# Kernel optimization log

Hardware: AMD Instinct MI355X
Metric: run time of the kernel (lower is better)

The kernel has to match this reference:

```python
import jax, jax.numpy as jnp
import numpy as np

B = 512          # number of (query, corpus) pairs
MAX_SET = 128    # max_set_size
D_IN, E_IN = 32, 16
D = 128          # node_state_dim == filters_3
E_ENC = 64
M_HID = 256
T_DIM = 128      # transform_dim
N_PROP = 5
SINKHORN_ITERS = 20
TEMP = 0.1
DEG = 8


def setup_inputs() -> dict:
    key = jax.random.key(0)
    ks = jax.random.split(key, 16)
    # alternating graph sizes: query 128/64, corpus 64/128
    qsizes = np.where(np.arange(B) % 2 == 0, 128, 64).astype(np.int32)
    csizes = np.where(np.arange(B) % 2 == 0, 64, 128).astype(np.int32)
    sizes_flat = np.stack([qsizes, csizes], 1).reshape(-1)        # [2B] interleaved q,c
    N = int(sizes_flat.sum())                                     # 98304
    E = DEG * N                                                   # 786432
    starts = np.concatenate([[0], np.cumsum(sizes_flat)[:-1]])
    graph_idx = np.repeat(np.arange(2 * B), sizes_flat).astype(np.int32)
    rng = np.random.default_rng(0)
    from_idx = rng.integers(0, N, E).astype(np.int64)
    g = graph_idx[from_idx]                                       # keep edges within a graph
    to_idx = (starts[g] + rng.integers(0, 1 << 30, E) % sizes_flat[g]).astype(np.int64)

    def W(k, shape):
        s = 1.0 / np.sqrt(shape[0])
        return jax.random.uniform(k, shape, jnp.float32, -s, s)

    return dict(
        node_features=jax.random.normal(ks[0], (N, D_IN), jnp.float32),
        edge_features=jax.random.normal(ks[1], (E, E_IN), jnp.float32),
        enc_node_w=W(ks[2], (D_IN, D)), enc_node_b=jnp.zeros((D,), jnp.float32),
        enc_edge_w=W(ks[3], (E_IN, E_ENC)), enc_edge_b=jnp.zeros((E_ENC,), jnp.float32),
        msg_w1=W(ks[4], (2 * D + E_ENC, M_HID)), msg_b1=jnp.zeros((M_HID,), jnp.float32),
        msg_w2=W(ks[5], (M_HID, D)), msg_b2=jnp.zeros((D,), jnp.float32),
        rmsg_w1=W(ks[6], (2 * D + E_ENC, M_HID)), rmsg_b1=jnp.zeros((M_HID,), jnp.float32),
        rmsg_w2=W(ks[7], (M_HID, D)), rmsg_b2=jnp.zeros((D,), jnp.float32),
        upd_w1=W(ks[8], (2 * D, M_HID)), upd_b1=jnp.zeros((M_HID,), jnp.float32),
        upd_w2=W(ks[9], (M_HID, D)), upd_b2=jnp.zeros((D,), jnp.float32),
        fc1_w=W(ks[10], (D, T_DIM)), fc1_b=jnp.zeros((T_DIM,), jnp.float32),
        fc2_w=W(ks[11], (T_DIM, T_DIM)), fc2_b=jnp.zeros((T_DIM,), jnp.float32),
        from_idx=jnp.asarray(from_idx, jnp.int32),
        to_idx=jnp.asarray(to_idx, jnp.int32),
        graph_idx=jnp.asarray(graph_idx, jnp.int32),
        qsizes=jnp.asarray(qsizes, jnp.int32),
        csizes=jnp.asarray(csizes, jnp.int32),
    )


def _mlp2(x, w1, b1, w2, b2):
    return jax.nn.relu(x @ w1 + b1) @ w2 + b2


def reference(node_features, edge_features, enc_node_w, enc_node_b, enc_edge_w, enc_edge_b,
              msg_w1, msg_b1, msg_w2, msg_b2, rmsg_w1, rmsg_b1, rmsg_w2, rmsg_b2,
              upd_w1, upd_b1, upd_w2, upd_b2, fc1_w, fc1_b, fc2_w, fc2_b,
              from_idx, to_idx, graph_idx, qsizes, csizes):
    N = node_features.shape[0]
    # GraphEncoder: linear MLPs on node / edge features
    h = node_features @ enc_node_w + enc_node_b                   # [N, D]
    e = edge_features @ enc_edge_w + enc_edge_b                   # [E, E_ENC]
    # GraphPropLayer applied n_prop_layers times (shared params)
    for _ in range(N_PROP):
        src, dst = h[from_idx], h[to_idx]
        m = _mlp2(jnp.concatenate([src, dst, e], -1), msg_w1, msg_b1, msg_w2, msg_b2)
        agg = jax.ops.segment_sum(m, to_idx, num_segments=N)
        mr = _mlp2(jnp.concatenate([dst, src, e], -1), rmsg_w1, rmsg_b1, rmsg_w2, rmsg_b2)
        agg = agg + jax.ops.segment_sum(mr, from_idx, num_segments=N)
        h = h + _mlp2(jnp.concatenate([agg, h], -1), upd_w1, upd_b1, upd_w2, upd_b2)
    # split into per-graph chunks and pad to MAX_SET (scatter by (pair, side, position))
    sizes_flat = jnp.stack([qsizes, csizes], 1).reshape(-1)       # [2B]
    starts = jnp.concatenate([jnp.zeros((1,), sizes_flat.dtype), jnp.cumsum(sizes_flat)[:-1]])
    pos = jnp.arange(N, dtype=jnp.int32) - starts[graph_idx]
    pair, side = graph_idx // 2, graph_idx % 2
    stacked = jnp.zeros((B, 2, MAX_SET, D), h.dtype).at[pair, side, pos].set(h)
    stacked_q, stacked_c = stacked[:, 0], stacked[:, 1]           # [B, MAX_SET, D]
    # masked transform
    tq = _mlp2(stacked_q, fc1_w, fc1_b, fc2_w, fc2_b)
    tc = _mlp2(stacked_c, fc1_w, fc1_b, fc2_w, fc2_b)
    ar = jnp.arange(MAX_SET)
    qmask = (ar[None, :] < qsizes[:, None]).astype(h.dtype)[:, :, None]
    cmask = (ar[None, :] < csizes[:, None]).astype(h.dtype)[:, :, None]
    mq, mc = qmask * tq, cmask * tc
    # sinkhorn (noise_factor = 0, temperature = 0.1, 20 iters)
    log_alpha = jnp.einsum('bqd,bcd->bqc', mq, mc) / TEMP         # [B, MAX_SET, MAX_SET]
    for _ in range(SINKHORN_ITERS):
        log_alpha = log_alpha - jax.scipy.special.logsumexp(log_alpha, axis=2, keepdims=True)
        log_alpha = log_alpha - jax.scipy.special.logsumexp(log_alpha, axis=1, keepdims=True)
    plan = jnp.exp(log_alpha)
    # masked residual score
    scores = -jnp.sum(jax.nn.relu(stacked_q - plan @ stacked_c), axis=(1, 2))  # [B]
    return scores
```

## Files before the change

kernel.cpp:

```cpp
#include <hip/hip_runtime.h>

using bf16x8 = __attribute__((ext_vector_type(8))) __bf16;
using u16x8  = __attribute__((ext_vector_type(8))) unsigned short;
using f32x4  = __attribute__((ext_vector_type(4))) float;
using f32x2  = __attribute__((ext_vector_type(2))) float;

#define DEV static __device__ __forceinline__

constexpr int NN = 98304;
constexpr int NE = 786432;
constexpr int NB = 512;

constexpr size_t OFF_HB  = 0;
constexpr size_t OFF_AGG = OFF_HB + (size_t)NN*128*2;
constexpr size_t OFF_TH  = OFF_AGG;
constexpr size_t OFF_TL  = OFF_AGG + (size_t)NN*128*2;
constexpr size_t OFF_W   = OFF_AGG + (size_t)NN*128*4;

constexpr size_t WO_W1TM = 0;
constexpr size_t WO_W1TR = WO_W1TM + (size_t)81920*2;
constexpr size_t WO_W2TM = WO_W1TR + (size_t)81920*2;
constexpr size_t WO_W2TR = WO_W2TM + (size_t)32768*2;
constexpr size_t WO_W1TU = WO_W2TR + (size_t)32768*2;
constexpr size_t WO_W2TU = WO_W1TU + (size_t)65536*2;
constexpr size_t WO_WNT  = WO_W2TU + (size_t)32768*2;
constexpr size_t WO_WETP = WO_WNT  + (size_t)4096*2;
constexpr size_t WO_FC1F = WO_WETP + (size_t)2048*2;
constexpr size_t WO_FC2F = WO_FC1F + (size_t)16384*4;
constexpr size_t WO_BNF  = WO_FC2F + (size_t)16384*4;
constexpr size_t WO_BEF  = WO_BNF + 128*4;
constexpr size_t WO_B1M  = WO_BEF + 64*4;
constexpr size_t WO_B2M  = WO_B1M + 256*4;
constexpr size_t WO_B1R  = WO_B2M + 128*4;
constexpr size_t WO_B2R  = WO_B1R + 256*4;
constexpr size_t WO_B1U  = WO_B2R + 128*4;
constexpr size_t WO_B2U  = WO_B1U + 256*4;
constexpr size_t WO_FC1B = WO_B2U + 128*4;
constexpr size_t WO_FC2B = WO_FC1B + 128*4;
constexpr size_t WO_FLAG = WO_FC2B + 128*4;
constexpr size_t WO_END  = WO_FLAG + 16;

constexpr size_t OFF_HL  = OFF_W + WO_END;
constexpr size_t WS_MINI = OFF_HL;
constexpr size_t WS_FULL = OFF_HL + (size_t)NN*128*2;

constexpr int    SCAN_CHUNKS= NN/256;
constexpr size_t CSR_INTS   = (size_t)2*(NN+1) + (size_t)2*NN + (size_t)2*NE + 768;
constexpr size_t CSR_BYTES  = CSR_INTS*4;
constexpr size_t WS_FULL_G  = WS_FULL + CSR_BYTES;
constexpr size_t WS_MINI_G  = WS_MINI + CSR_BYTES;

DEV unsigned short f2bf(float f){
  unsigned u = __float_as_uint(f);
  u += 0x7fffu + ((u >> 16) & 1u);
  return (unsigned short)(u >> 16);
}
DEV float bf2f(unsigned short s){ return __uint_as_float(((unsigned)s) << 16); }

DEV unsigned short ldbf(const void* p, size_t i, int fl){
  return fl ? ((const unsigned short*)p)[i] : f2bf(((const float*)p)[i]);
}
DEV float ldf(const void* p, size_t i, int fl){
  return fl ? bf2f(((const unsigned short*)p)[i]) : ((const float*)p)[i];
}

DEV f32x4 mfma16(u16x8 a, u16x8 b, f32x4 c){
  bf16x8 A, B;
  __builtin_memcpy(&A, &a, 16);
  __builtin_memcpy(&B, &b, 16);
  return __builtin_amdgcn_mfma_f32_16x16x32_bf16(A, B, c, 0, 0, 0);
}

__global__ void k_dtype(const unsigned short* nf_u16, int* flag){
  if (threadIdx.x != 0 || blockIdx.x != 0) return;
  int sane = 0;
  for (int i = 0; i < 64; ++i){
    unsigned short v = nf_u16[2*i];
    int e = (v >> 7) & 0xFF;
    if (e >= 0x70 && e <= 0x8E) sane++;
  }
  *flag = (sane >= 32) ? 1 : 0;
}

__global__ void k_sent(float* out){
  int i = blockIdx.x*256 + threadIdx.x;
  if (i < NB) out[i] = 10000.f;
}

__global__ void k_canary(void* out, const int* flag){
  int i = blockIdx.x*256 + threadIdx.x;
  if (i < NB){
    if (*flag) ((unsigned short*)out)[i] = (unsigned short)0x4580u;
    else       ((float*)out)[i] = 4096.f;
  }
}

__global__ void k_zero(float* agg){
  f32x4* p = (f32x4*)agg;
  int gtid = blockIdx.x*256 + threadIdx.x;
  for (int i = gtid; i < NN*128/4; i += 786432){
    f32x4 z = {0.f, 0.f, 0.f, 0.f};
    p[i] = z;
  }
}

__global__ void k_prep(
  const void* enc_node_w, const void* enc_node_b,
  const void* enc_edge_w, const void* enc_edge_b,
  const void* msg_w1, const void* msg_b1,
  const void* msg_w2, const void* msg_b2,
  const void* rmsg_w1, const void* rmsg_b1,
  const void* rmsg_w2, const void* rmsg_b2,
  const void* upd_w1, const void* upd_b1,
  const void* upd_w2, const void* upd_b2,
  const void* fc1_w, const void* fc1_b,
  const void* fc2_w, const void* fc2_b,
  char* wsb)
{
  int fl = *(const int*)(wsb + OFF_W + WO_FLAG);
  int i = blockIdx.x*256 + threadIdx.x;
  unsigned short* W1Tm = (unsigned short*)(wsb + OFF_W + WO_W1TM);
  unsigned short* W1Tr = (unsigned short*)(wsb + OFF_W + WO_W1TR);
  unsigned short* W2Tm = (unsigned short*)(wsb + OFF_W + WO_W2TM);
  unsigned short* W2Tr = (unsigned short*)(wsb + OFF_W + WO_W2TR);
  unsigned short* W1Tu = (unsigned short*)(wsb + OFF_W + WO_W1TU);
  unsigned short* W2Tu = (unsigned short*)(wsb + OFF_W + WO_W2TU);
  unsigned short* WnT  = (unsigned short*)(wsb + OFF_W + WO_WNT);
  unsigned short* WeTp = (unsigned short*)(wsb + OFF_W + WO_WETP);
  float* fc1f = (float*)(wsb + OFF_W + WO_FC1F);
  float* fc2f = (float*)(wsb + OFF_W + WO_FC2F);
  float* bnf  = (float*)(wsb + OFF_W + WO_BNF);
  float* bef  = (float*)(wsb + OFF_W + WO_BEF);
  float* b1m  = (float*)(wsb + OFF_W + WO_B1M);
  float* b2m  = (float*)(wsb + OFF_W + WO_B2M);
  float* b1r  = (float*)(wsb + OFF_W + WO_B1R);
  float* b2r  = (float*)(wsb + OFF_W + WO_B2R);
  float* b1u  = (float*)(wsb + OFF_W + WO_B1U);
  float* b2u  = (float*)(wsb + OFF_W + WO_B2U);
  float* f1b  = (float*)(wsb + OFF_W + WO_FC1B);
  float* f2b  = (float*)(wsb + OFF_W + WO_FC2B);

  if (i < 81920){ W1Tm[i] = ldbf(msg_w1,  (size_t)(i%320)*256 + (i/320), fl); return; } i -= 81920;
  if (i < 81920){ W1Tr[i] = ldbf(rmsg_w1, (size_t)(i%320)*256 + (i/320), fl); return; } i -= 81920;
  if (i < 32768){ W2Tm[i] = ldbf(msg_w2,  (size_t)(i%256)*128 + (i/256), fl); return; } i -= 32768;
  if (i < 32768){ W2Tr[i] = ldbf(rmsg_w2, (size_t)(i%256)*128 + (i/256), fl); return; } i -= 32768;
  if (i < 65536){ W1Tu[i] = ldbf(upd_w1,  (size_t)(i%256)*256 + (i/256), fl); return; } i -= 65536;
  if (i < 32768){ W2Tu[i] = ldbf(upd_w2,  (size_t)(i%256)*128 + (i/256), fl); return; } i -= 32768;
  if (i <  4096){ WnT[i]  = ldbf(enc_node_w, (size_t)(i%32)*128 + (i/32), fl); return; } i -= 4096;
  if (i <  2048){ int k = i%32, n = i/32;
                  WeTp[i] = (k<16) ? ldbf(enc_edge_w, (size_t)k*64 + n, fl) : (unsigned short)0; return; } i -= 2048;
  if (i < 16384){ fc1f[i] = ldf(fc1_w, i, fl); return; } i -= 16384;
  if (i < 16384){ fc2f[i] = ldf(fc2_w, i, fl); return; } i -= 16384;
  if (i <   128){ bnf[i] = ldf(enc_node_b, i, fl); return; } i -= 128;
  if (i <    64){ bef[i] = ldf(enc_edge_b, i, fl); return; } i -= 64;
  if (i <   256){ b1m[i] = ldf(msg_b1, i, fl); return; } i -= 256;
  if (i <   128){ b2m[i] = ldf(msg_b2, i, fl); return; } i -= 128;
  if (i <   256){ b1r[i] = ldf(rmsg_b1, i, fl); return; } i -= 256;
  if (i <   128){ b2r[i] = ldf(rmsg_b2, i, fl); return; } i -= 128;
  if (i <   256){ b1u[i] = ldf(upd_b1, i, fl); return; } i -= 256;
  if (i <   128){ b2u[i] = ldf(upd_b2, i, fl); return; } i -= 128;
  if (i <   128){ f1b[i] = ldf(fc1_b, i, fl); return; } i -= 128;
  if (i <   128){ f2b[i] = ldf(fc2_b, i, fl); return; }
}

__global__ void k_csr_zero(int* cur0, int* cur1){
  int i = blockIdx.x*256 + threadIdx.x;
  if (i < NN){ cur0[i] = 0; cur1[i] = 0; }
}
__global__ void k_csr_count(const int* from_idx, const int* to_idx, int* cur0, int* cur1){
  int e = blockIdx.x*256 + threadIdx.x;
  if (e < NE){
    atomicAdd(&cur0[to_idx[e]], 1);
    atomicAdd(&cur1[from_idx[e]], 1);
  }
}
__global__ void k_scan1(const int* cur0, const int* cur1, int* csum){
  __shared__ int red[256];
  int b = blockIdx.x, tid = threadIdx.x;
  const int* c = (b >= SCAN_CHUNKS) ? cur1 : cur0;
  int cb = (b >= SCAN_CHUNKS) ? (b - SCAN_CHUNKS) : b;
  red[tid] = c[cb*256 + tid];
  __syncthreads();
  for (int off = 128; off > 0; off >>= 1){
    if (tid < off) red[tid] += red[tid + off];
    __syncthreads();
  }
  if (tid == 0) csum[b] = red[0];
}
__global__ void k_scan2(int* csum, int* offs0, int* offs1){
  int wv = threadIdx.x >> 6, lane = threadIdx.x & 63;
  if (wv >= 2) return;
  int basei = wv * SCAN_CHUNKS;
  int carry = 0;
  for (int j = 0; j < SCAN_CHUNKS/64; ++j){
    int x = csum[basei + j*64 + lane];
    int s = x;
    for (int off = 1; off < 64; off <<= 1){
      int t = __shfl_up(s, off, 64);
      if (lane >= off) s += t;
    }
    csum[basei + j*64 + lane] = s - x + carry;
    carry += __shfl(s, 63, 64);
  }
  if (lane == 0){
    if (wv == 0) offs0[NN] = carry; else offs1[NN] = carry;
  }
}
__global__ void k_scan3(int* cur0, int* cur1, const int* csum, int* offs0, int* offs1){
  __shared__ int s[256];
  int b = blockIdx.x, tid = threadIdx.x;
  int dir = (b >= SCAN_CHUNKS) ? 1 : 0;
  int cb  = dir ? (b - SCAN_CHUNKS) : b;
  int* c    = dir ? cur1 : cur0;
  int* offs = dir ? offs1 : offs0;
  int v = c[cb*256 + tid];
  s[tid] = v;
  __syncthreads();
  for (int off = 1; off < 256; off <<= 1){
    int t = (tid >= off) ? s[tid - off] : 0;
    __syncthreads();
    s[tid] += t;
    __syncthreads();
  }
  int excl = s[tid] - v + csum[b];
  offs[cb*256 + tid] = excl;
  c[cb*256 + tid] = excl;
}
__global__ void k_csr_fill(const int* from_idx, const int* to_idx,
                           int* cur0, int* cur1, int* ent0, int* ent1){
  int e = blockIdx.x*256 + threadIdx.x;
  if (e < NE){
    int p0 = atomicAdd(&cur0[to_idx[e]], 1);   ent0[p0] = e;
    int p1 = atomicAdd(&cur1[from_idx[e]], 1); ent1[p1] = e;
  }
}

__global__ void __launch_bounds__(256) k_enc_node(
  const void* nf, const unsigned short* wnt, const float* bnf,
  unsigned short* hb, unsigned short* hl, int has_hl, const int* flag)
{
  int fl = *flag;
  const u16x8* wnt8 = (const u16x8*)wnt;
  int tid = threadIdx.x, wv = tid>>6, lane = tid&63, quad = lane>>4, l15 = lane&15;
  int n0 = blockIdx.x*64;
  f32x4 acc[4][2];
  for (int a=0;a<4;a++){ f32x4 z = {0.f,0.f,0.f,0.f}; acc[a][0]=z; acc[a][1]=z; }
  u16x8 av[4], bv[2];
  if (fl){
    const u16x8* nf8 = (const u16x8*)nf;
    for (int mt=0; mt<4; ++mt) av[mt] = nf8[(size_t)(n0 + mt*16 + l15)*4 + quad];
  } else {
    const float* nff = (const float*)nf;
    for (int mt=0; mt<4; ++mt){
      const float* rp = nff + (size_t)(n0 + mt*16 + l15)*32 + quad*8;
      u16x8 v;
      for (int j=0;j<8;j++) v[j] = f2bf(rp[j]);
      av[mt] = v;
    }
  }
  for (int nt=0; nt<2; ++nt) bv[nt] = wnt8[(size_t)(wv*32 + nt*16 + l15)*4 + quad];
  for (int mt=0; mt<4; ++mt)
    for (int nt=0; nt<2; ++nt)
      acc[mt][nt] = mfma16(av[mt], bv[nt], acc[mt][nt]);
  for (int mt=0; mt<4; ++mt)
    for (int nt=0; nt<2; ++nt){
      int n = wv*32 + nt*16 + l15;
      float bias = bnf[n];
      for (int r=0;r<4;r++){
        int m = mt*16 + quad*4 + r;
        float v = acc[mt][nt][r] + bias;
        size_t idx = (size_t)(n0+m)*128 + n;
        unsigned short hi = f2bf(v);
        hb[idx] = hi;
        if (has_hl) hl[idx] = f2bf(v - bf2f(hi));
      }
    }
}

__global__ void __launch_bounds__(256) k_msg(
  const unsigned short* hbg, const void* efg,
  const int* from_idx, const int* to_idx,
  const unsigned short* w1tm, const unsigned short* w1tr,
  const unsigned short* w2tm, const unsigned short* w2tr,
  const unsigned short* wetp, const float* bef,
  const float* b1m, const float* b2m, const float* b1r, const float* b2r,
  float* agg, const int* flag)
{
  __shared__ __align__(16) unsigned short XsB[40*32*8];
  __shared__ __align__(16) unsigned short HsB[32*32*8];
  __shared__ int fromS[32], toS[32];
  int fl = *flag;
  u16x8* Xs = (u16x8*)XsB;
  u16x8* Hs = (u16x8*)HsB;
  const u16x8* hb8   = (const u16x8*)hbg;
  const u16x8* wetp8 = (const u16x8*)wetp;
  const u16x8* w1tm8 = (const u16x8*)w1tm;
  const u16x8* w1tr8 = (const u16x8*)w1tr;
  const u16x8* w2tm8 = (const u16x8*)w2tm;
  const u16x8* w2tr8 = (const u16x8*)w2tr;

  int tid = threadIdx.x;
  int e0 = blockIdx.x*32;
  if (tid < 32) fromS[tid] = from_idx[e0 + tid];
  else if (tid < 64) toS[tid-32] = to_idx[e0 + tid - 32];
  __syncthreads();
  int m = tid & 31, g = tid >> 5;
  int wv = tid>>6, lane = tid&63, quad = lane>>4, l15 = lane&15;
  u16x8 zero8 = {0,0,0,0,0,0,0,0};

  for (int j=0; j<4; ++j){
    int kb = g + 8*j;
    u16x8 v = (kb < 16) ? hb8[(size_t)fromS[m]*16 + kb]
                        : hb8[(size_t)toS[m]*16 + (kb-16)];
    Xs[kb*32 + m] = v;
  }
  {
    f32x4 accE[2];
    for (int a=0;a<2;a++){ f32x4 z = {0.f,0.f,0.f,0.f}; accE[a]=z; }
    u16x8 bvE = wetp8[(size_t)(wv*16 + l15)*4 + quad];
    for (int mt=0; mt<2; ++mt){
      u16x8 avE = zero8;
      if (quad < 2){
        if (fl){
          avE = ((const u16x8*)efg)[(size_t)(e0 + mt*16 + l15)*2 + quad];
        } else {
          const float* ep = (const float*)efg + (size_t)(e0 + mt*16 + l15)*16 + quad*8;
          u16x8 v;
          for (int j=0;j<8;j++) v[j] = f2bf(ep[j]);
          avE = v;
        }
      }
      accE[mt] = mfma16(avE, bvE, accE[mt]);
    }
    int n = wv*16 + l15;
    float bias = bef[n];
    for (int mt=0; mt<2; ++mt)
      for (int r=0;r<4;r++){
        int me = mt*16 + quad*4 + r;
        XsB[((32 + (n>>3))*32 + me)*8 + (n&7)] = f2bf(accE[mt][r] + bias);
      }
  }
  __syncthreads();

  for (int dir=0; dir<2; ++dir){
    const u16x8* W1T = dir ? w1tr8 : w1tm8;
    const u16x8* W2T = dir ? w2tr8 : w2tm8;
    const float* B1  = dir ? b1r : b1m;
    const float* B2  = dir ? b2r : b2m;
    f32x4 acc1[2][4];
    for (int a=0;a<2;a++)
      for (int b=0;b<4;b++){ f32x4 z = {0.f,0.f,0.f,0.f}; acc1[a][b]=z; }
    for (int ks=0; ks<10; ++ks){
      u16x8 bv[4], av[2];
      for (int nt=0; nt<4; ++nt)
        bv[nt] = W1T[(size_t)(wv*64 + nt*16 + l15)*40 + ks*4 + quad];
      int kb = ks*4 + quad;
      int kbm = dir ? (kb < 32 ? (kb ^ 16) : kb) : kb;
      for (int mt=0; mt<2; ++mt)
        av[mt] = Xs[kbm*32 + mt*16 + l15];
      for (int mt=0; mt<2; ++mt)
        for (int nt=0; nt<4; ++nt)
          acc1[mt][nt] = mfma16(av[mt], bv[nt], acc1[mt][nt]);
    }
    __syncthreads();
    for (int mt=0; mt<2; ++mt)
      for (int nt=0; nt<4; ++nt){
        int n = wv*64 + nt*16 + l15;
        float bias = B1[n];
        for (int r=0;r<4;r++){
          int mm = mt*16 + quad*4 + r;
          float v = fmaxf(acc1[mt][nt][r] + bias, 0.f);
          HsB[((n>>3)*32 + mm)*8 + (n&7)] = f2bf(v);
        }
      }
    __syncthreads();
    f32x4 acc2[2][2];
    for (int a=0;a<2;a++)
      for (int b=0;b<2;b++){ f32x4 z = {0.f,0.f,0.f,0.f}; acc2[a][b]=z; }
    for (int ks=0; ks<8; ++ks){
      u16x8 bv[2], av[2];
      for (int nt=0; nt<2; ++nt)
        bv[nt] = W2T[(size_t)(wv*32 + nt*16 + l15)*32 + ks*4 + quad];
      for (int mt=0; mt<2; ++mt)
        av[mt] = Hs[(ks*4 + quad)*32 + mt*16 + l15];
      for (int mt=0; mt<2; ++mt)
        for (int nt=0; nt<2; ++nt)
          acc2[mt][nt] = mfma16(av[mt], bv[nt], acc2[mt][nt]);
    }
    for (int mt=0; mt<2; ++mt)
      for (int nt=0; nt<2; ++nt){
        int n = wv*32 + nt*16 + l15;
        float bias = B2[n];
        for (int r=0;r<4;r++){
          int mm = mt*16 + quad*4 + r;
          int row = dir ? fromS[mm] : toS[mm];
          atomicAdd(agg + (size_t)row*128 + n, acc2[mt][nt][r] + bias);
        }
      }
  }
}

__global__ void __launch_bounds__(512, 4) k_msg11(
  const unsigned short* hbg, const void* efg,
  const int* from_idx, const int* to_idx,
  const int* ent0, const int* ent1,
  const unsigned short* w1tm, const unsigned short* w1tr,
  const unsigned short* w2tm, const unsigned short* w2tr,
  const unsigned short* wetp, const float* bef,
  const float* b1m, const float* b2m, const float* b1r, const float* b2r,
  float* agg, const int* flag)
{
  __shared__ __align__(16) unsigned short XsB[40*64*8];
  __shared__ __align__(16) unsigned short HsB[32*64*8];
  __shared__ int eS[64], oS[64], tS[64];
  __shared__ int runBeg[65];
  __shared__ int nRunsS;
  int fl = *flag;
  u16x8* Xs = (u16x8*)XsB;
  u16x8* Hs = (u16x8*)HsB;
  const u16x8* hb8   = (const u16x8*)hbg;
  const u16x8* wetp8 = (const u16x8*)wetp;
  const u16x8* w1tm8 = (const u16x8*)w1tm;
  const u16x8* w1tr8 = (const u16x8*)w1tr;
  const u16x8* w2tm8 = (const u16x8*)w2tm;
  const u16x8* w2tr8 = (const u16x8*)w2tr;

  int tid = threadIdx.x;
  int cpx = (int)gridDim.x >> 3;
  int bb = ((int)blockIdx.x & 7) * cpx + ((int)blockIdx.x >> 3);
  int e0 = bb * 64;
  int w = tid>>6, lane = tid&63, quad = lane>>4, l15 = lane&15;
  u16x8 zero8 = {0,0,0,0,0,0,0,0};

  for (int part = 0; part < 2; ++part){
    const int* ent   = part ? ent1 : ent0;
    const int* oidx  = part ? to_idx : from_idx;
    const int* tidx  = part ? from_idx : to_idx;
    const u16x8* W1T = part ? w1tr8 : w1tm8;
    const u16x8* W2T = part ? w2tr8 : w2tm8;
    const float* B1  = part ? b1r : b1m;
    const float* B2  = part ? b2r : b2m;

    __syncthreads();
    if (tid < 64){
      int e = ent[e0 + tid];
      eS[tid] = e;
      oS[tid] = oidx[e];
      tS[tid] = tidx[e];
    }
    __syncthreads();
    if (tid == 0){
      int nr = 0;
      for (int mm=0; mm<64; ++mm)
        if (mm==0 || tS[mm]!=tS[mm-1]) runBeg[nr++] = mm;
      runBeg[nr] = 64; nRunsS = nr;
    }
    {
      int edge = tid & 63, cg = tid >> 6;
      for (int j=0; j<4; ++j){
        int kb = cg + 8*j;
        u16x8 v = (kb < 16) ? hb8[(size_t)oS[edge]*16 + kb]
                            : hb8[(size_t)tS[edge]*16 + (kb-16)];
        Xs[kb*64 + edge] = v;
      }
    }
    {
      int wm = w >> 2, wn = w & 3;
      f32x4 accE[2];
      for (int a=0;a<2;a++){ f32x4 z = {0.f,0.f,0.f,0.f}; accE[a]=z; }
      u16x8 bvE = wetp8[(size_t)(wn*16 + l15)*4 + quad];
      for (int mt=0; mt<2; ++mt){
        u16x8 avE = zero8;
        if (quad < 2){
          int e = eS[wm*32 + mt*16 + l15];
          if (fl){
            avE = ((const u16x8*)efg)[(size_t)e*2 + quad];
          } else {
            const float* ep = (const float*)efg + (size_t)e*16 + quad*8;
            u16x8 v;
            for (int j=0;j<8;j++) v[j] = f2bf(ep[j]);
            avE = v;
          }
        }
        accE[mt] = mfma16(avE, bvE, accE[mt]);
      }
      int n = wn*16 + l15;
      float bias = bef[n];
      for (int mt=0; mt<2; ++mt)
        for (int r=0;r<4;r++){
          int me = wm*32 + mt*16 + quad*4 + r;
          XsB[((32 + (n>>3))*64 + me)*8 + (n&7)] = f2bf(accE[mt][r] + bias);
        }
    }
    __syncthreads();

    f32x4 acc1[4][2];
    for (int a=0;a<4;a++)
      for (int b=0;b<2;b++){ f32x4 z = {0.f,0.f,0.f,0.f}; acc1[a][b]=z; }
    for (int ks=0; ks<10; ++ks){
      u16x8 bv[2], av[4];
      for (int nt=0; nt<2; ++nt)
        bv[nt] = W1T[(size_t)(w*32 + nt*16 + l15)*40 + ks*4 + quad];
      int kb = ks*4 + quad;
      for (int mt=0; mt<4; ++mt)
        av[mt] = Xs[kb*64 + mt*16 + l15];
      for (int mt=0; mt<4; ++mt)
        for (int nt=0; nt<2; ++nt)
          acc1[mt][nt] = mfma16(av[mt], bv[nt], acc1[mt][nt]);
    }
    for (int mt=0; mt<4; ++mt)
      for (int nt=0; nt<2; ++nt){
        int n = w*32 + nt*16 + l15;
        float bias = B1[n];
        for (int r=0;r<4;r++){
          int mm = mt*16 + quad*4 + r;
          float v = fmaxf(acc1[mt][nt][r] + bias, 0.f);
          HsB[((n>>3)*64 + mm)*8 + (n&7)] = f2bf(v);
        }
      }
    __syncthreads();
    f32x4 acc2[4];
    for (int a=0;a<4;a++){ f32x4 z = {0.f,0.f,0.f,0.f}; acc2[a]=z; }
    int n2 = w*16 + l15;
    for (int ks=0; ks<8; ++ks){
      u16x8 bv1 = W2T[(size_t)n2*32 + ks*4 + quad];
      u16x8 av[4];
      for (int mt=0; mt<4; ++mt)
        av[mt] = Hs[(ks*4 + quad)*64 + mt*16 + l15];
      for (int mt=0; mt<4; ++mt)
        acc2[mt] = mfma16(av[mt], bv1, acc2[mt]);
    }
    __syncthreads();
    float* P = (float*)HsB;
    {
      float bias = B2[n2];
      for (int mt=0; mt<4; ++mt)
        for (int r=0;r<4;r++){
          int mm = mt*16 + quad*4 + r;
          P[mm*128 + n2] = acc2[mt][r] + bias;
        }
    }
    __syncthreads();
    {
      int col = tid & 127, grp = tid >> 7;
      int nr = nRunsS;
      for (int k = grp; k < nr; k += 4){
        int r0 = runBeg[k], r1 = runBeg[k+1];
        float s = 0.f;
        for (int mm = r0; mm < r1; ++mm) s += P[mm*128 + col];
        atomicAdd(agg + (size_t)tS[r0]*128 + col, s);
      }
    }
  }
}

__global__ void __launch_bounds__(512, 4) k_upd(
  float* agg, const unsigned short* hbg,
  const unsigned short* w1tu, const unsigned short* w2tu,
  const float* b1u, const float* b2u,
  unsigned short* hb, unsigned short* hl, int has_hl)
{
  __shared__ __align__(16) unsigned short XsB[32*64*8];
  __shared__ __align__(16) unsigned short HsB[32*64*8];
  u16x8* Xs = (u16x8*)XsB;
  u16x8* Hs = (u16x8*)HsB;
  const u16x8* hb8   = (const u16x8*)hbg;
  const u16x8* w1tu8 = (const u16x8*)w1tu;
  const u16x8* w2tu8 = (const u16x8*)w2tu;
  int tid = threadIdx.x;
  int n0 = blockIdx.x*64;
  {
    int node = tid & 63, cg = tid >> 6;
    for (int j=0; j<4; ++j){
      int kb = cg + 8*j;
      u16x8 v;
      if (kb < 16){
        const float* ap = agg + (size_t)(n0+node)*128 + kb*8;
        for (int t=0;t<8;t++) v[t] = f2bf(ap[t]);
      } else {
        v = hb8[(size_t)(n0+node)*16 + (kb-16)];
      }
      Xs[kb*64 + node] = v;
    }
  }
  __syncthreads();
  {
    f32x4* ap4 = (f32x4*)(agg + (size_t)n0*128);
    f32x4 z = {0.f,0.f,0.f,0.f};
    for (int i = tid; i < 64*128/4; i += 512) ap4[i] = z;
  }
  int w = tid>>6, lane = tid&63, quad = lane>>4, l15 = lane&15;
  f32x4 acc1[4][2];
  for (int a=0;a<4;a++)
    for (int b=0;b<2;b++){ f32x4 z = {0.f,0.f,0.f,0.f}; acc1[a][b]=z; }
  for (int ks=0; ks<8; ++ks){
    u16x8 bv[2], av[4];
    for (int nt=0; nt<2; ++nt)
      bv[nt] = w1tu8[(size_t)(w*32 + nt*16 + l15)*32 + ks*4 + quad];
    for (int mt=0; mt<4; ++mt)
      av[mt] = Xs[(ks*4 + quad)*64 + mt*16 + l15];
    for (int mt=0; mt<4; ++mt)
      for (int nt=0; nt<2; ++nt)
        acc1[mt][nt] = mfma16(av[mt], bv[nt], acc1[mt][nt]);
  }
  __syncthreads();
  for (int mt=0; mt<4; ++mt)
    for (int nt=0; nt<2; ++nt){
      int n = w*32 + nt*16 + l15;
      float bias = b1u[n];
      for (int r=0;r<4;r++){
        int mm = mt*16 + quad*4 + r;
        float v = fmaxf(acc1[mt][nt][r] + bias, 0.f);
        HsB[((n>>3)*64 + mm)*8 + (n&7)] = f2bf(v);
      }
    }
  __syncthreads();
  f32x4 acc2[4];
  for (int a=0;a<4;a++){ f32x4 z = {0.f,0.f,0.f,0.f}; acc2[a]=z; }
  int n2 = w*16 + l15;
  for (int ks=0; ks<8; ++ks){
    u16x8 bv2 = w2tu8[(size_t)n2*32 + ks*4 + quad];
    u16x8 av[4];
    for (int mt=0; mt<4; ++mt)
      av[mt] = Hs[(ks*4 + quad)*64 + mt*16 + l15];
    for (int mt=0; mt<4; ++mt)
      acc2[mt] = mfma16(av[mt], bv2, acc2[mt]);
  }
  float bias = b2u[n2];
  for (int mt=0; mt<4; ++mt)
    for (int r=0;r<4;r++){
      int mm = mt*16 + quad*4 + r;
      size_t idx = (size_t)(n0+mm)*128 + n2;
      float base = bf2f(hb[idx]);
      if (has_hl) base += bf2f(hl[idx]);
      float nv = base + acc2[mt][r] + bias;
      unsigned short hi = f2bf(nv);
      hb[idx] = hi;
      if (has_hl) hl[idx] = f2bf(nv - bf2f(hi));
    }
}

__global__ void __launch_bounds__(256) k_tmlp(
  const unsigned short* hb, const unsigned short* hl, int has_hl,
  const float* fc1f, const float* fc2f,
  const float* fc1b, const float* fc2b, unsigned short* Th, unsigned short* Tl)
{
  __shared__ float Xs[16][128];
  __shared__ float Hsm[16][128];
  int tid = threadIdx.x, wv = tid>>6, lane = tid&63;
  int nodeBase = blockIdx.x*16 + wv*4;
  for (int i=0;i<4;i++){
    size_t base = (size_t)(nodeBase+i)*128 + lane*2;
    float x0 = bf2f(hb[base]), x1 = bf2f(hb[base+1]);
    if (has_hl){ x0 += bf2f(hl[base]); x1 += bf2f(hl[base+1]); }
    Xs[wv*4+i][lane*2] = x0; Xs[wv*4+i][lane*2+1] = x1;
  }
  __syncthreads();
  float a0[4], a1[4];
  for (int i=0;i<4;i++){ a0[i] = fc1b[lane*2]; a1[i] = fc1b[lane*2+1]; }
  for (int k=0;k<128;k++){
    f32x2 w = *(const f32x2*)&fc1f[k*128 + lane*2];
    for (int i=0;i<4;i++){ float x = Xs[wv*4+i][k]; a0[i] += x*w[0]; a1[i] += x*w[1]; }
  }
  for (int i=0;i<4;i++){
    Hsm[wv*4+i][lane*2]   = fmaxf(a0[i], 0.f);
    Hsm[wv*4+i][lane*2+1] = fmaxf(a1[i], 0.f);
  }
  __syncthreads();
  for (int i=0;i<4;i++){ a0[i] = fc2b[lane*2]; a1[i] = fc2b[lane*2+1]; }
  for (int k=0;k<128;k++){
    f32x2 w = *(const f32x2*)&fc2f[k*128 + lane*2];
    for (int i=0;i<4;i++){ float x = Hsm[wv*4+i][k]; a0[i] += x*w[0]; a1[i] += x*w[1]; }
  }
  for (int i=0;i<4;i++){
    size_t idx = (size_t)(nodeBase+i)*128 + lane*2;
    float t0 = a0[i], t1 = a1[i];
    unsigned short h0 = f2bf(t0), h1 = f2bf(t1);
    Th[idx] = h0; Th[idx+1] = h1;
    Tl[idx]   = f2bf(t0 - bf2f(h0));
    Tl[idx+1] = f2bf(t1 - bf2f(h1));
  }
}

__global__ void __launch_bounds__(256) k_pair(
  const unsigned short* Th, const unsigned short* Tl,
  const unsigned short* hb, const unsigned short* hl, int has_hl,
  void* outv, const int* flag)
{
  __shared__ float la[8448];
  __shared__ float red[4];
  const u16x8* th8 = (const u16x8*)Th;
  const u16x8* tl8 = (const u16x8*)Tl;
  int b = blockIdx.x;
  int even = ((b & 1) == 0);
  int qs = even ? 128 : 64;
  int cs = 192 - qs;
  int nr = even ? 128 : 65;
  int nc = even ? 65 : 128;
  int st = nc + 1;
  int q0 = 192*b, c0 = q0 + qs;
  int tid = threadIdx.x, wv = tid>>6, lane = tid&63, quad = lane>>4, l15 = lane&15;
  u16x8 zero8 = {0,0,0,0,0,0,0,0};

  f32x4 acc[2][8];
  for (int a=0;a<2;a++)
    for (int c=0;c<8;c++){ f32x4 z = {0.f,0.f,0.f,0.f}; acc[a][c]=z; }
  for (int pass=0; pass<3; ++pass){
    const u16x8* A  = (pass==2) ? tl8 : th8;
    const u16x8* Bm = (pass==1) ? tl8 : th8;
    for (int ks=0; ks<4; ++ks){
      u16x8 av[2], bv[8];
      for (int mt=0; mt<2; ++mt){
        int q = wv*32 + mt*16 + l15;
        av[mt] = (q < qs) ? A[(size_t)(q0+q)*16 + ks*4 + quad] : zero8;
      }
      for (int nt=0; nt<8; ++nt){
        int c = nt*16 + l15;
        bv[nt] = (c < cs) ? Bm[(size_t)(c0+c)*16 + ks*4 + quad] : zero8;
      }
      for (int mt=0; mt<2; ++mt)
        for (int nt=0; nt<8; ++nt)
          acc[mt][nt] = mfma16(av[mt], bv[nt], acc[mt][nt]);
    }
  }
  for (int mt=0; mt<2; ++mt)
    for (int nt=0; nt<8; ++nt)
      for (int r=0;r<4;r++){
        int q = wv*32 + mt*16 + quad*4 + r;
        int c = nt*16 + l15;
        if (q < nr && c < nc) la[q*st + c] = acc[mt][nt][r] * 10.0f;
      }
  __syncthreads();

  for (int it=0; it<20; ++it){
    if (tid < nr){
      float* row = &la[tid*st];
      float mx = -1e30f;
      for (int c=0;c<nc;c++) mx = fmaxf(mx, row[c]);
      float s = 0.f, last = 0.f;
      for (int c=0;c<nc;c++){ float e = __expf(row[c]-mx); s += e; last = e; }
      if (even) s += 63.f * last;
      float l = mx + __logf(s);
      for (int c=0;c<nc;c++) row[c] -= l;
    }
    __syncthreads();
    if (tid < nc){
      int c = tid;
      float mx = -1e30f;
      for (int r=0;r<nr;r++) mx = fmaxf(mx, la[r*st + c]);
      float s = 0.f, last = 0.f;
      for (int r=0;r<nr;r++){ float e = __expf(la[r*st + c]-mx); s += e; last = e; }
      if (!even) s += 63.f * last;
      float l = mx + __logf(s);
      for (int r=0;r<nr;r++) la[r*st + c] -= l;
    }
    __syncthreads();
  }
  for (int i = tid; i < 8448; i += 256) la[i] = __expf(la[i]);
  __syncthreads();

  int d = tid & 127, qg = tid >> 7;
  int nsweep = (nr + 15) >> 4;
  float partial = 0.f;
  for (int sweep=0; sweep<nsweep; ++sweep){
    int qb = sweep*16 + qg*8;
    float acc2[8];
    for (int j=0;j<8;j++) acc2[j] = 0.f;
    for (int c=0; c<cs; ++c){
      size_t si = (size_t)(c0+c)*128 + d;
      float s = bf2f(hb[si]);
      if (has_hl) s += bf2f(hl[si]);
      for (int j=0;j<8;j++){
        int r = qb + j;
        if (r < nr) acc2[j] += la[r*st + c] * s;
      }
    }
    for (int j=0;j<8;j++){
      int r = qb + j;
      if (r < nr){
        float w = (!even && r == 64) ? 64.f : 1.f;
        float sq = 0.f;
        if (r < qs){
          size_t si = (size_t)(q0+r)*128 + d;
          sq = bf2f(hb[si]);
          if (has_hl) sq += bf2f(hl[si]);
        }
        partial += w * fmaxf(sq - acc2[j], 0.f);
      }
    }
  }
  for (int off=32; off>0; off>>=1) partial += __shfl_down(partial, off, 64);
  if (lane == 0) red[wv] = partial;
  __syncthreads();
  if (tid == 0){
    float tot = red[0] + red[1] + red[2] + red[3];
    if (*flag) ((unsigned short*)outv)[b] = f2bf(-tot);
    else       ((float*)outv)[b] = -tot;
  }
}

extern "C" void kernel_launch(void* const* d_in, const int* in_sizes, int n_in,
                              void* d_out, int out_size, void* d_ws, size_t ws_size,
                              hipStream_t stream)
{
  if (ws_size < WS_MINI){
    k_sent<<<2, 256, 0, stream>>>((float*)d_out);
    return;
  }
  int has_hl = 0, use_s = 0;
  size_t off_csr = 0;
  if (ws_size >= WS_FULL_G){ has_hl = 1; use_s = 1; off_csr = WS_FULL; }
  else if (ws_size >= WS_FULL){ has_hl = 1; use_s = 0; }
  else if (ws_size >= WS_MINI_G){ has_hl = 0; use_s = 1; off_csr = WS_MINI; }

  const int* from_idx = (const int*)d_in[22];
  const int* to_idx   = (const int*)d_in[23];

  char* wsb = (char*)d_ws;
  unsigned short* hb  = (unsigned short*)(wsb + OFF_HB);
  unsigned short* hl  = (unsigned short*)(wsb + OFF_HL);
  float* agg          = (float*)(wsb + OFF_AGG);
  unsigned short* Th  = (unsigned short*)(wsb + OFF_TH);
  unsigned short* Tl  = (unsigned short*)(wsb + OFF_TL);
  int* flag           = (int*)(wsb + OFF_W + WO_FLAG);

  const unsigned short* w1tm = (const unsigned short*)(wsb + OFF_W + WO_W1TM);
  const unsigned short* w1tr = (const unsigned short*)(wsb + OFF_W + WO_W1TR);
  const unsigned short* w2tm = (const unsigned short*)(wsb + OFF_W + WO_W2TM);
  const unsigned short* w2tr = (const unsigned short*)(wsb + OFF_W + WO_W2TR);
  const unsigned short* w1tu = (const unsigned short*)(wsb + OFF_W + WO_W1TU);
  const unsigned short* w2tu = (const unsigned short*)(wsb + OFF_W + WO_W2TU);
  const unsigned short* wnt  = (const unsigned short*)(wsb + OFF_W + WO_WNT);
  const unsigned short* wetp = (const unsigned short*)(wsb + OFF_W + WO_WETP);
  const float* fc1f  = (const float*)(wsb + OFF_W + WO_FC1F);
  const float* fc2f  = (const float*)(wsb + OFF_W + WO_FC2F);
  const float* bnf   = (const float*)(wsb + OFF_W + WO_BNF);
  const float* bef   = (const float*)(wsb + OFF_W + WO_BEF);
  const float* b1m   = (const float*)(wsb + OFF_W + WO_B1M);
  const float* b2m   = (const float*)(wsb + OFF_W + WO_B2M);
  const float* b1r   = (const float*)(wsb + OFF_W + WO_B1R);
  const float* b2r   = (const float*)(wsb + OFF_W + WO_B2R);
  const float* b1u   = (const float*)(wsb + OFF_W + WO_B1U);
  const float* b2u   = (const float*)(wsb + OFF_W + WO_B2U);
  const float* f1b   = (const float*)(wsb + OFF_W + WO_FC1B);
  const float* f2b   = (const float*)(wsb + OFF_W + WO_FC2B);

  int* offs0 = (int*)(wsb + off_csr);
  int* offs1 = offs0 + (NN + 1);
  int* cur0  = offs1 + (NN + 1);
  int* cur1  = cur0 + NN;
  int* ent0  = cur1 + NN;
  int* ent1  = ent0 + NE;
  int* csum  = ent1 + NE;

  k_dtype<<<1, 64, 0, stream>>>((const unsigned short*)d_in[0], flag);

  k_canary<<<2, 256, 0, stream>>>(d_out, flag);

  k_prep<<<1439, 256, 0, stream>>>(
    d_in[2],  d_in[3],  d_in[4],  d_in[5],
    d_in[6],  d_in[7],  d_in[8],  d_in[9],
    d_in[10], d_in[11], d_in[12], d_in[13],
    d_in[14], d_in[15], d_in[16], d_in[17],
    d_in[18], d_in[19], d_in[20], d_in[21],
    wsb);

  if (use_s){
    k_csr_zero <<<NN/256, 256, 0, stream>>>(cur0, cur1);
    k_csr_count<<<NE/256, 256, 0, stream>>>(from_idx, to_idx, cur0, cur1);
    k_scan1    <<<2*SCAN_CHUNKS, 256, 0, stream>>>(cur0, cur1, csum);
    k_scan2    <<<1, 128, 0, stream>>>(csum, offs0, offs1);
    k_scan3    <<<2*SCAN_CHUNKS, 256, 0, stream>>>(cur0, cur1, csum, offs0, offs1);
    k_csr_fill <<<NE/256, 256, 0, stream>>>(from_idx, to_idx, cur0, cur1, ent0, ent1);
  }

  k_enc_node<<<NN/64, 256, 0, stream>>>(d_in[0], wnt, bnf, hb, hl, has_hl, flag);

  k_zero<<<3072, 256, 0, stream>>>(agg);
  for (int r=0; r<5; ++r){
    if (use_s){
      k_msg11<<<NE/64, 512, 0, stream>>>(hb, d_in[1],
          from_idx, to_idx, ent0, ent1,
          w1tm, w1tr, w2tm, w2tr, wetp, bef,
          b1m, b2m, b1r, b2r, agg, flag);
    } else {
      k_msg<<<NE/32, 256, 0, stream>>>(hb, d_in[1],
          from_idx, to_idx, w1tm, w1tr, w2tm, w2tr, wetp, bef,
          b1m, b2m, b1r, b2r, agg, flag);
    }
    k_upd<<<NN/64, 512, 0, stream>>>(agg, hb, w1tu, w2tu, b1u, b2u, hb, hl, has_hl);
  }

  k_tmlp<<<NN/16, 256, 0, stream>>>(hb, hl, has_hl, fc1f, fc2f, f1b, f2b, Th, Tl);
  k_pair<<<NB, 256, 0, stream>>>(Th, Tl, hb, hl, has_hl, d_out, flag);
}
```

Measured before the change: 6.181 ms.

## Share gathered edge inputs between both message directions and pad LDS rows

The message kernel now gathers each edge tile once, from ent0 sorted by destination, and runs both the forward and reverse MLPs on it. The reverse direction reuses the same LDS tile by swapping the from/to halves through index remapping, which removes a second gather of node states and edge features. Forward results are reduced over runs of equal destination before the atomic add. Reverse results are atomically added per edge, which means more scattered atomics. LDS row stride is padded from 64 to 65 to reduce bank conflicts, and the update kernel loads agg with vector loads.

After: 5.832 ms. 1.06x faster.

```diff
diff --git a/kernel.cpp b/kernel.cpp
--- a/kernel.cpp
+++ b/kernel.cpp
@@ -49,6 +49,8 @@
 constexpr size_t CSR_BYTES  = CSR_INTS*4;
 constexpr size_t WS_FULL_G  = WS_FULL + CSR_BYTES;
 constexpr size_t WS_MINI_G  = WS_MINI + CSR_BYTES;
+
+constexpr int LP = 65;
 
 DEV unsigned short f2bf(float f){
   unsigned u = __float_as_uint(f);
@@ -400,19 +402,18 @@
   }
 }
 
-__global__ void __launch_bounds__(512, 4) k_msg11(
+__global__ void __launch_bounds__(512, 4) k_msg8(
   const unsigned short* hbg, const void* efg,
-  const int* from_idx, const int* to_idx,
-  const int* ent0, const int* ent1,
+  const int* from_idx, const int* to_idx, const int* ent,
   const unsigned short* w1tm, const unsigned short* w1tr,
   const unsigned short* w2tm, const unsigned short* w2tr,
   const unsigned short* wetp, const float* bef,
   const float* b1m, const float* b2m, const float* b1r, const float* b2r,
   float* agg, const int* flag)
 {
-  __shared__ __align__(16) unsigned short XsB[40*64*8];
-  __shared__ __align__(16) unsigned short HsB[32*64*8];
-  __shared__ int eS[64], oS[64], tS[64];
+  __shared__ __align__(16) unsigned short XsB[40*LP*8];
+  __shared__ __align__(16) unsigned short HsB[32*LP*8];
+  __shared__ int eS[64], fromS[64], toS[64];
   __shared__ int runBeg[65];
   __shared__ int nRunsS;
   int fl = *flag;
@@ -429,71 +430,65 @@
   int cpx = (int)gridDim.x >> 3;
   int bb = ((int)blockIdx.x & 7) * cpx + ((int)blockIdx.x >> 3);
   int e0 = bb * 64;
+  if (tid < 64){
+    int e = ent[e0 + tid];
+    eS[tid] = e;
+    fromS[tid] = from_idx[e];
+    toS[tid]   = to_idx[e];
+  }
+  __syncthreads();
   int w = tid>>6, lane = tid&63, quad = lane>>4, l15 = lane&15;
   u16x8 zero8 = {0,0,0,0,0,0,0,0};
 
-  for (int part = 0; part < 2; ++part){
-    const int* ent   = part ? ent1 : ent0;
-    const int* oidx  = part ? to_idx : from_idx;
-    const int* tidx  = part ? from_idx : to_idx;
-    const u16x8* W1T = part ? w1tr8 : w1tm8;
-    const u16x8* W2T = part ? w2tr8 : w2tm8;
-    const float* B1  = part ? b1r : b1m;
-    const float* B2  = part ? b2r : b2m;
-
-    __syncthreads();
-    if (tid < 64){
-      int e = ent[e0 + tid];
-      eS[tid] = e;
-      oS[tid] = oidx[e];
-      tS[tid] = tidx[e];
-    }
-    __syncthreads();
-    if (tid == 0){
-      int nr = 0;
-      for (int mm=0; mm<64; ++mm)
-        if (mm==0 || tS[mm]!=tS[mm-1]) runBeg[nr++] = mm;
-      runBeg[nr] = 64; nRunsS = nr;
-    }
-    {
-      int edge = tid & 63, cg = tid >> 6;
-      for (int j=0; j<4; ++j){
-        int kb = cg + 8*j;
-        u16x8 v = (kb < 16) ? hb8[(size_t)oS[edge]*16 + kb]
-                            : hb8[(size_t)tS[edge]*16 + (kb-16)];
-        Xs[kb*64 + edge] = v;
-      }
-    }
-    {
-      int wm = w >> 2, wn = w & 3;
-      f32x4 accE[2];
-      for (int a=0;a<2;a++){ f32x4 z = {0.f,0.f,0.f,0.f}; accE[a]=z; }
-      u16x8 bvE = wetp8[(size_t)(wn*16 + l15)*4 + quad];
-      for (int mt=0; mt<2; ++mt){
-        u16x8 avE = zero8;
-        if (quad < 2){
-          int e = eS[wm*32 + mt*16 + l15];
-          if (fl){
-            avE = ((const u16x8*)efg)[(size_t)e*2 + quad];
-          } else {
-            const float* ep = (const float*)efg + (size_t)e*16 + quad*8;
-            u16x8 v;
-            for (int j=0;j<8;j++) v[j] = f2bf(ep[j]);
-            avE = v;
-          }
+  if (tid == 0){
+    int nr = 0;
+    for (int mm=0; mm<64; ++mm)
+      if (mm==0 || toS[mm]!=toS[mm-1]) runBeg[nr++] = mm;
+    runBeg[nr] = 64; nRunsS = nr;
+  }
+  {
+    int edge = tid & 63, cg = tid >> 6;
+    for (int j=0; j<4; ++j){
+      int kb = cg + 8*j;
+      u16x8 v = (kb < 16) ? hb8[(size_t)fromS[edge]*16 + kb]
+                          : hb8[(size_t)toS[edge]*16 + (kb-16)];
+      Xs[kb*LP + edge] = v;
+    }
+  }
+  {
+    int wm = w >> 2, wn = w & 3;
+    f32x4 accE[2];
+    for (int a=0;a<2;a++){ f32x4 z = {0.f,0.f,0.f,0.f}; accE[a]=z; }
+    u16x8 bvE = wetp8[(size_t)(wn*16 + l15)*4 + quad];
+    for (int mt=0; mt<2; ++mt){
+      u16x8 avE = zero8;
+      if (quad < 2){
+        int e = eS[wm*32 + mt*16 + l15];
+        if (fl){
+          avE = ((const u16x8*)efg)[(size_t)e*2 + quad];
+        } else {
+          const float* ep = (const float*)efg + (size_t)e*16 + quad*8;
+          u16x8 v;
+          for (int j=0;j<8;j++) v[j] = f2bf(ep[j]);
+          avE = v;
         }
-        accE[mt] = mfma16(avE, bvE, accE[mt]);
-      }
-      int n = wn*16 + l15;
-      float bias = bef[n];
-      for (int mt=0; mt<2; ++mt)
-        for (int r=0;r<4;r++){
-          int me = wm*32 + mt*16 + quad*4 + r;
-          XsB[((32 + (n>>3))*64 + me)*8 + (n&7)] = f2bf(accE[mt][r] + bias);
-        }
-    }
-    __syncthreads();
-
+      }
+      accE[mt] = mfma16(avE, bvE, accE[mt]);
+    }
+    int n = wn*16 + l15;
+    float bias = bef[n];
+    for (int mt=0; mt<2; ++mt)
+      for (int r=0;r<4;r++){
+        int me = wm*32 + mt*16 + quad*4 + r;
+        XsB[((32 + (n>>3))*LP + me)*8 + (n&7)] = f2bf(accE[mt][r] + bias);
+      }
+  }
+  __syncthreads();
+
+  for (int dir=0; dir<2; ++dir){
+    const u16x8* W1T = dir ? w1tr8 : w1tm8;
+    const u16x8* W2T = dir ? w2tr8 : w2tm8;
+    const float* B1  = dir ? b1r : b1m;
     f32x4 acc1[4][2];
     for (int a=0;a<4;a++)
       for (int b=0;b<2;b++){ f32x4 z = {0.f,0.f,0.f,0.f}; acc1[a][b]=z; }
@@ -502,12 +497,14 @@
       for (int nt=0; nt<2; ++nt)
         bv[nt] = W1T[(size_t)(w*32 + nt*16 + l15)*40 + ks*4 + quad];
       int kb = ks*4 + quad;
+      int kbm = dir ? (kb < 32 ? (kb ^ 16) : kb) : kb;
       for (int mt=0; mt<4; ++mt)
-        av[mt] = Xs[kb*64 + mt*16 + l15];
+        av[mt] = Xs[kbm*LP + mt*16 + l15];
       for (int mt=0; mt<4; ++mt)
         for (int nt=0; nt<2; ++nt)
           acc1[mt][nt] = mfma16(av[mt], bv[nt], acc1[mt][nt]);
     }
+    if (dir == 1) __syncthreads();
     for (int mt=0; mt<4; ++mt)
       for (int nt=0; nt<2; ++nt){
         int n = w*32 + nt*16 + l15;
@@ -515,7 +512,7 @@
         for (int r=0;r<4;r++){
           int mm = mt*16 + quad*4 + r;
           float v = fmaxf(acc1[mt][nt][r] + bias, 0.f);
-          HsB[((n>>3)*64 + mm)*8 + (n&7)] = f2bf(v);
+          HsB[((n>>3)*LP + mm)*8 + (n&7)] = f2bf(v);
         }
       }
     __syncthreads();
@@ -526,30 +523,35 @@
       u16x8 bv1 = W2T[(size_t)n2*32 + ks*4 + quad];
       u16x8 av[4];
       for (int mt=0; mt<4; ++mt)
-        av[mt] = Hs[(ks*4 + quad)*64 + mt*16 + l15];
+        av[mt] = Hs[(ks*4 + quad)*LP + mt*16 + l15];
       for (int mt=0; mt<4; ++mt)
         acc2[mt] = mfma16(av[mt], bv1, acc2[mt]);
     }
-    __syncthreads();
-    float* P = (float*)HsB;
-    {
-      float bias = B2[n2];
+    if (dir == 0){
+      __syncthreads();
+      float* P = (float*)HsB;
+      float bias = b2m[n2];
       for (int mt=0; mt<4; ++mt)
         for (int r=0;r<4;r++){
           int mm = mt*16 + quad*4 + r;
           P[mm*128 + n2] = acc2[mt][r] + bias;
         }
-    }
-    __syncthreads();
-    {
+      __syncthreads();
       int col = tid & 127, grp = tid >> 7;
       int nr = nRunsS;
       for (int k = grp; k < nr; k += 4){
         int r0 = runBeg[k], r1 = runBeg[k+1];
         float s = 0.f;
         for (int mm = r0; mm < r1; ++mm) s += P[mm*128 + col];
-        atomicAdd(agg + (size_t)tS[r0]*128 + col, s);
-      }
+        atomicAdd(agg + (size_t)toS[r0]*128 + col, s);
+      }
+    } else {
+      float bias = b2r[n2];
+      for (int mt=0; mt<4; ++mt)
+        for (int r=0;r<4;r++){
+          int mm = mt*16 + quad*4 + r;
+          atomicAdd(agg + (size_t)fromS[mm]*128 + n2, acc2[mt][r] + bias);
+        }
     }
   }
 }
@@ -560,8 +562,8 @@
   const float* b1u, const float* b2u,
   unsigned short* hb, unsigned short* hl, int has_hl)
 {
-  __shared__ __align__(16) unsigned short XsB[32*64*8];
-  __shared__ __align__(16) unsigned short HsB[32*64*8];
+  __shared__ __align__(16) unsigned short XsB[32*LP*8];
+  __shared__ __align__(16) unsigned short HsB[32*LP*8];
   u16x8* Xs = (u16x8*)XsB;
   u16x8* Hs = (u16x8*)HsB;
   const u16x8* hb8   = (const u16x8*)hbg;
@@ -575,12 +577,14 @@
       int kb = cg + 8*j;
       u16x8 v;
       if (kb < 16){
-        const float* ap = agg + (size_t)(n0+node)*128 + kb*8;
-        for (int t=0;t<8;t++) v[t] = f2bf(ap[t]);
+        const f32x4* ap = (const f32x4*)(agg + (size_t)(n0+node)*128 + kb*8);
+        f32x4 a0 = ap[0], a1 = ap[1];
+        v[0]=f2bf(a0[0]); v[1]=f2bf(a0[1]); v[2]=f2bf(a0[2]); v[3]=f2bf(a0[3]);
+        v[4]=f2bf(a1[0]); v[5]=f2bf(a1[1]); v[6]=f2bf(a1[2]); v[7]=f2bf(a1[3]);
       } else {
         v = hb8[(size_t)(n0+node)*16 + (kb-16)];
       }
-      Xs[kb*64 + node] = v;
+      Xs[kb*LP + node] = v;
     }
   }
   __syncthreads();
@@ -598,7 +602,7 @@
     for (int nt=0; nt<2; ++nt)
       bv[nt] = w1tu8[(size_t)(w*32 + nt*16 + l15)*32 + ks*4 + quad];
     for (int mt=0; mt<4; ++mt)
-      av[mt] = Xs[(ks*4 + quad)*64 + mt*16 + l15];
+      av[mt] = Xs[(ks*4 + quad)*LP + mt*16 + l15];
     for (int mt=0; mt<4; ++mt)
       for (int nt=0; nt<2; ++nt)
         acc1[mt][nt] = mfma16(av[mt], bv[nt], acc1[mt][nt]);
@@ -611,7 +615,7 @@
       for (int r=0;r<4;r++){
         int mm = mt*16 + quad*4 + r;
         float v = fmaxf(acc1[mt][nt][r] + bias, 0.f);
-        HsB[((n>>3)*64 + mm)*8 + (n&7)] = f2bf(v);
+        HsB[((n>>3)*LP + mm)*8 + (n&7)] = f2bf(v);
       }
     }
   __syncthreads();
@@ -622,7 +626,7 @@
     u16x8 bv2 = w2tu8[(size_t)n2*32 + ks*4 + quad];
     u16x8 av[4];
     for (int mt=0; mt<4; ++mt)
-      av[mt] = Hs[(ks*4 + quad)*64 + mt*16 + l15];
+      av[mt] = Hs[(ks*4 + quad)*LP + mt*16 + l15];
     for (int mt=0; mt<4; ++mt)
       acc2[mt] = mfma16(av[mt], bv2, acc2[mt]);
   }
@@ -879,9 +883,8 @@
   k_zero<<<3072, 256, 0, stream>>>(agg);
   for (int r=0; r<5; ++r){
     if (use_s){
-      k_msg11<<<NE/64, 512, 0, stream>>>(hb, d_in[1],
-          from_idx, to_idx, ent0, ent1,
-          w1tm, w1tr, w2tm, w2tr, wetp, bef,
+      k_msg8<<<NE/64, 512, 0, stream>>>(hb, d_in[1],
+          from_idx, to_idx, ent0, w1tm, w1tr, w2tm, w2tr, wetp, bef,
           b1m, b2m, b1r, b2r, agg, flag);
     } else {
       k_msg<<<NE/32, 256, 0, stream>>>(hb, d_in[1],
```
